# Optimization experiments

Measured on AMD Instinct MI355X. Metric: run time of the kernel, lower is better.

The kernel has to match this reference:

```python
import jax, jax.numpy as jnp
import numpy as np

B, N, D_IN = 4, 2048, 128
H, HD = 4, 32  # num_heads, head_dim (out_features=128, concat=True)
NEG_SLOPE = 0.2


def setup_inputs() -> dict:
    key = jax.random.key(0)
    kx, kadj, kw, ka = jax.random.split(key, 4)
    x = jax.random.normal(kx, (B, N, D_IN), dtype=jnp.float32)
    adj_mx = jax.random.randint(kadj, (N, N), 0, 2, dtype=jnp.int32)
    # xavier-uniform-ish scaling for params
    W = jax.random.normal(kw, (H * HD, D_IN), dtype=jnp.float32) * (1.0 / np.sqrt(D_IN))
    a = jax.random.normal(ka, (H, 2 * HD, 1), dtype=jnp.float32) * (1.0 / np.sqrt(2 * HD))
    return {"x": x, "adj_mx": adj_mx, "W": W, "a": a}


def reference(x, adj_mx, W, a):
    # x: (B,N,D_in); W: (H*hd, D_in) [nn.Linear weight]; a: (H, 2*hd, 1)
    b, n, _ = x.shape
    hd = a.shape[1] // 2
    h = (x @ W.T).reshape(b, n, H, hd)  # (B,N,H,hd)
    # e_ij = a^T [h_i || h_j] = a1.h_i + a2.h_j  (exact decomposition of the concat-matmul)
    a1 = a[:, :hd, 0]  # (H, hd)
    a2 = a[:, hd:, 0]  # (H, hd)
    ei = jnp.einsum('bnhd,hd->bnh', h, a1)
    ej = jnp.einsum('bnhd,hd->bnh', h, a2)
    e = ei[:, :, None, :] + ej[:, None, :, :]  # (B,N,N,H)
    e = jnp.where(e > 0, e, NEG_SLOPE * e)  # leaky_relu(0.2)
    mask = (adj_mx == 0)[None, :, :, None]  # (1,N,N,1)
    e = jnp.where(mask, -jnp.inf, e)
    attn = jax.nn.softmax(e, axis=2)  # softmax over neighbors j
    # dropout p=0.0 (inference) -> identity
    out = jnp.einsum('bijh,bjhd->bihd', attn, h)  # (B,N,H,hd)
    return out.reshape(b, n, H * hd)  # concat heads
```

## Files before the change

### kernel.cpp

```cpp
#include <hip/hip_runtime.h>
#include <hip/hip_bf16.h>
#include <stdint.h>

#define B 4
#define N 2048
#define DIN 128
#define H 4
#define HD 32
#define NEG 0.2f
#define LOG2E 1.4426950408889634f
#define WINJ 256

typedef __attribute__((ext_vector_type(8))) short short8;
typedef __attribute__((ext_vector_type(4))) float f32x4;


__global__ __launch_bounds__(256) void k_prep(const float* __restrict__ x,
                                              const float* __restrict__ W,
                                              const float* __restrict__ a,
                                              const int* __restrict__ adj,
                                              unsigned short* __restrict__ VT,
                                              float* __restrict__ ei_t,
                                              float* __restrict__ ej_t,
                                              unsigned long long* __restrict__ bitsT) {
    __shared__ float Wt0[64][64];
    __shared__ float Wt1[64][64];
    __shared__ float xT[64][20];

    const int tid = threadIdx.x;
    if (blockIdx.x >= 512) {
        int t = (blockIdx.x - 512) * 256 + tid;
        int v = adj[t];
        unsigned long long m = __ballot(v != 0);
        if ((tid & 63) == 0) {
            int row = t >> 11, jw = (t >> 6) & 31;
            bitsT[(size_t)jw * 2048 + row] = m;
        }
        return;
    }

    const int lane = tid & 63;
    const int r0 = (tid >> 6) * 4;
    const int c2 = lane;
    const int rowBase = blockIdx.x * 16;
    float acc[4][2];
#pragma unroll
    for (int i = 0; i < 4; ++i) { acc[i][0] = 0.f; acc[i][1] = 0.f; }

    for (int kh = 0; kh < 2; ++kh) {
        __syncthreads();
        {
            const int c = tid & 127;
            const int qb = (tid >> 7) * 8;
            const int ci = c >> 1, pl = c & 1;
            const float4* W4 = (const float4*)W;
#pragma unroll
            for (int q = 0; q < 8; ++q) {
                float4 v = W4[c * 32 + kh * 16 + qb + q];
                int kk = (qb + q) * 4;
                if (pl == 0) {
                    Wt0[kk + 0][ci] = v.x; Wt0[kk + 1][ci] = v.y;
                    Wt0[kk + 2][ci] = v.z; Wt0[kk + 3][ci] = v.w;
                } else {
                    Wt1[kk + 0][ci] = v.x; Wt1[kk + 1][ci] = v.y;
                    Wt1[kk + 2][ci] = v.z; Wt1[kk + 3][ci] = v.w;
                }
            }
        }
        {
            const int rl = tid >> 4;
            const int q = tid & 15;
            float4 v = ((const float4*)x)[(rowBase + rl) * 32 + kh * 16 + q];
            int kk = q * 4;
            xT[kk + 0][rl] = v.x; xT[kk + 1][rl] = v.y;
            xT[kk + 2][rl] = v.z; xT[kk + 3][rl] = v.w;
        }
        __syncthreads();
#pragma unroll 8
        for (int kk = 0; kk < 64; ++kk) {
            float w0 = Wt0[kk][c2];
            float w1 = Wt1[kk][c2];
#pragma unroll
            for (int i = 0; i < 4; ++i) {
                float xv = xT[kk][r0 + i];
                acc[i][0] += xv * w0;
                acc[i][1] += xv * w1;
            }
        }
    }

    const int c0 = 2 * c2;
    const int headT = c0 >> 5, d0 = c0 & 31;
    const int b = rowBase >> 11;
    const int n0 = (rowBase & 2047) + r0;
    const int bh = b * 4 + headT;

    {
        ushort4 p0, p1;
        unsigned short* q0 = (unsigned short*)&p0;
        unsigned short* q1 = (unsigned short*)&p1;
#pragma unroll
        for (int i = 0; i < 4; ++i) {
            __hip_bfloat16 h0 = __float2bfloat16(acc[i][0]);
            __hip_bfloat16 h1 = __float2bfloat16(acc[i][1]);
            q0[i] = *(unsigned short*)&h0;
            q1[i] = *(unsigned short*)&h1;
        }
        const int wdw = n0 >> 8;
        const int gw  = (n0 >> 3) & 31;
        const int off = n0 & 7;
        const int gs0 = gw ^ (d0 & 7);
        const int gs1 = gw ^ ((d0 + 1) & 7);
        *(ushort4*)&VT[((size_t)bh * 32 + d0) * 2048 + wdw * WINJ + gs0 * 8 + off] = p0;
        *(ushort4*)&VT[((size_t)bh * 32 + d0 + 1) * 2048 + wdw * WINJ + gs1 * 8 + off] = p1;
    }
    {
        float a10 = a[headT * 64 + d0],      a11 = a[headT * 64 + d0 + 1];
        float a20 = a[headT * 64 + 32 + d0], a21 = a[headT * 64 + 32 + d0 + 1];
#pragma unroll
        for (int i = 0; i < 4; ++i) {
            float pi = acc[i][0] * a10 + acc[i][1] * a11;
            float pj = acc[i][0] * a20 + acc[i][1] * a21;
#pragma unroll
            for (int off = 1; off < 16; off <<= 1) {
                pi += __shfl_xor(pi, off);
                pj += __shfl_xor(pj, off);
            }
            if ((lane & 15) == 0) {
                ei_t[(size_t)bh * 2048 + n0 + i] = pi * LOG2E;
                ej_t[(size_t)bh * 2048 + n0 + i] = pj * LOG2E;
            }
        }
    }
}

__global__ __launch_bounds__(256) void k_attn_w(const unsigned short* __restrict__ VT,
                                                const float* __restrict__ ei_t,
                                                const float* __restrict__ ej_t,
                                                const unsigned long long* __restrict__ bitsT,
                                                float* __restrict__ out) {
    __shared__ __align__(16) unsigned short Vs[2][32 * WINJ];
    __shared__ __align__(16) float ejs[2][WINJ];

    const int tid = threadIdx.x;
    const int bid = blockIdx.x;
    const int rt = bid & 31;
    const int head = (bid >> 5) & 3;
    const int b = bid >> 7;
    const int wv = tid >> 6, lane = tid & 63;
    const int lr = lane & 15;
    const int g = lane >> 4;
    const int rowW = rt * 64 + wv * 16;
    const int bh = b * 4 + head;

    const unsigned short* VTb = VT + (size_t)bh * 32 * 2048;
    const float* ejg = ej_t + (size_t)bh * 2048;
    const float eir = ei_t[(size_t)bh * 2048 + rowW + lr];

    f32x4 acc0 = {0.f, 0.f, 0.f, 0.f};
    f32x4 acc1 = {0.f, 0.f, 0.f, 0.f};
    f32x4 accS = {0.f, 0.f, 0.f, 0.f};
    short8 onesb;
    {
        short ov = (lr == 0) ? (short)0x3F80 : (short)0;
#pragma unroll
        for (int e = 0; e < 8; ++e) onesb[e] = ov;
    }

    {
#pragma unroll
        for (int i = 0; i < 4; ++i) {
            int L = i * 256 + tid, d = L >> 5, gr = L & 31;
            float4 v = *(const float4*)&VTb[(size_t)d * 2048 + gr * 8];
            *(float4*)&Vs[0][(size_t)L * 8] = v;
        }
        if (tid < 64) {
            float4 e = *(const float4*)&ejg[tid * 4];
            *(float4*)&ejs[0][tid * 4] = e;
        }
    }
    __syncthreads();

    for (int w = 0; w < 8; ++w) {
        const int buf = w & 1;
        const unsigned long long wreg =
            bitsT[(size_t)(w * 4 + g) * 2048 + rowW + lr];

        float4 vr0, vr1, vr2, vr3, er;
        const bool pf = (w < 7);
        if (pf) {
            const unsigned short* src = VTb + (w + 1) * WINJ;
            vr0 = *(const float4*)&src[(size_t)((tid)        >> 5) * 2048 + ((tid)        & 31) * 8];
            vr1 = *(const float4*)&src[(size_t)((256 + tid)  >> 5) * 2048 + ((256 + tid)  & 31) * 8];
            vr2 = *(const float4*)&src[(size_t)((512 + tid)  >> 5) * 2048 + ((512 + tid)  & 31) * 8];
            vr3 = *(const float4*)&src[(size_t)((768 + tid)  >> 5) * 2048 + ((768 + tid)  & 31) * 8];
            if (tid < 64) er = *(const float4*)&ejg[(w + 1) * WINJ + tid * 4];
        }
        __builtin_amdgcn_sched_barrier(0);

        const unsigned short* Vb = &Vs[buf][0];
        const float* ejb = &ejs[buf][0];
#pragma unroll
        for (int jl = 0; jl < WINJ; jl += 64) {
            const unsigned long long word = __shfl(wreg, (jl >> 6) * 16 + lr);
#pragma unroll
            for (int ks = 0; ks < 2; ++ks) {
                const int gw_ = (jl >> 3) + ks * 4 + g;
                const int slot = gw_ ^ (lr & 7);
                short8 b0 = *(const short8*)&Vb[lr * WINJ + slot * 8];
                short8 b1 = *(const short8*)&Vb[(16 + lr) * WINJ + slot * 8];
                const int f = jl + ks * 32 + g * 8;
                float4 ea = *(const float4*)&ejb[f];
                float4 eb = *(const float4*)&ejb[f + 4];
                const unsigned int mb =
                    (unsigned int)(word >> (ks * 32 + g * 8)) & 0xffu;
                float ej8[8] = {ea.x, ea.y, ea.z, ea.w, eb.x, eb.y, eb.z, eb.w};
                short8 pa;
#pragma unroll
                for (int e = 0; e < 8; ++e) {
                    float s = eir + ej8[e];
                    float el = fmaxf(s, NEG * s);
                    float p = ((mb >> e) & 1u) ? __builtin_amdgcn_exp2f(el) : 0.f;
                    __hip_bfloat16 pb = __float2bfloat16(p);
                    pa[e] = (short)*(unsigned short*)&pb;
                }
                __builtin_amdgcn_s_setprio(1);
                acc0 = __builtin_amdgcn_mfma_f32_16x16x32_bf16(pa, b0, acc0, 0, 0, 0);
                acc1 = __builtin_amdgcn_mfma_f32_16x16x32_bf16(pa, b1, acc1, 0, 0, 0);
                accS = __builtin_amdgcn_mfma_f32_16x16x32_bf16(pa, onesb, accS, 0, 0, 0);
                __builtin_amdgcn_s_setprio(0);
            }
        }

        if (pf) {
            const int nbuf = buf ^ 1;
            *(float4*)&Vs[nbuf][(size_t)tid * 8]          = vr0;
            *(float4*)&Vs[nbuf][(size_t)(256 + tid) * 8]  = vr1;
            *(float4*)&Vs[nbuf][(size_t)(512 + tid) * 8]  = vr2;
            *(float4*)&Vs[nbuf][(size_t)(768 + tid) * 8]  = vr3;
            if (tid < 64) *(float4*)&ejs[nbuf][tid * 4] = er;
        }
        __syncthreads();
    }

#pragma unroll
    for (int reg = 0; reg < 4; ++reg) {
        const float sr = __shfl(accS[reg], g * 16);
        const float inv = 1.f / sr;
        const int m = 4 * g + reg;
        float* dst = &out[(size_t)(b * N + rowW + m) * 128 + head * 32 + lr];
        dst[0]  = acc0[reg] * inv;
        dst[16] = acc1[reg] * inv;
    }
}

__global__ __launch_bounds__(256) void k_fused(const float* __restrict__ x,
                                               const int* __restrict__ adj,
                                               const float* __restrict__ W,
                                               const float* __restrict__ a,
                                               float* __restrict__ out) {
    __shared__ float Ws[32][129];
    __shared__ float xs[64][132];
    __shared__ float hs[64][44];
    __shared__ float ejs[64];
    __shared__ float eis[128];
    __shared__ float a1s[32], a2s[32];
    __shared__ unsigned long long mb[128];

    const int tid = threadIdx.x;
    const int bid = blockIdx.x;
    const int rt = bid & 15;
    const int head = (bid >> 4) & 3;
    const int b = bid >> 6;
    const int row0 = rt * 128;

    for (int idx = tid; idx < 32 * 128; idx += 256) {
        int d = idx >> 7, k = idx & 127;
        Ws[d][k] = W[(head * 32 + d) * 128 + k];
    }
    if (tid < 32) a1s[tid] = a[head * 64 + tid];
    else if (tid < 64) a2s[tid - 32] = a[head * 64 + tid];
    __syncthreads();

    for (int c0 = 0; c0 < 128; c0 += 64) {
        __syncthreads();
        {
            int jj = tid >> 2, k0 = (tid & 3) * 32;
            const float4* src = (const float4*)&x[(b * N + row0 + c0 + jj) * 128 + k0];
#pragma unroll
            for (int q = 0; q < 8; ++q) *(float4*)&xs[jj][k0 + q * 4] = src[q];
        }
        __syncthreads();
        {
            int jj = tid >> 2, db = (tid & 3) * 8;
#pragma unroll
            for (int dd = 0; dd < 8; ++dd) {
                float s = 0.f;
                for (int k = 0; k < 128; ++k) s += xs[jj][k] * Ws[db + dd][k];
                hs[jj][db + dd] = s;
            }
        }
        __syncthreads();
        if (tid < 64) {
            float s = 0.f;
#pragma unroll
            for (int d = 0; d < 32; ++d) s += hs[tid][d] * a1s[d];
            eis[c0 + tid] = s;
        }
    }

    const int dgrp = tid & 3, d0 = dgrp * 8;
    const int rseg = tid >> 2;
    float acc[2][8];
    float sacc[2] = {0.f, 0.f};
#pragma unroll
    for (int k = 0; k < 2; ++k)
#pragma unroll
        for (int d = 0; d < 8; ++d) acc[k][d] = 0.f;

    for (int jc = 0; jc < N; jc += 64) {
        __syncthreads();
        {
            int jj = tid >> 2, k0 = (tid & 3) * 32;
            const float4* src = (const float4*)&x[(b * N + jc + jj) * 128 + k0];
#pragma unroll
            for (int q = 0; q < 8; ++q) *(float4*)&xs[jj][k0 + q * 4] = src[q];
        }
        {
            int wv = tid >> 6, lane = tid & 63;
            for (int p = 0; p < 32; ++p) {
                int il = p * 4 + wv;
                unsigned long long m = __ballot(adj[(row0 + il) * N + jc + lane] != 0);
                if (lane == 0) mb[il] = m;
            }
        }
        __syncthreads();
        {
            int jj = tid >> 2, db = (tid & 3) * 8;
#pragma unroll
            for (int dd = 0; dd < 8; ++dd) {
                float s = 0.f;
                for (int k = 0; k < 128; ++k) s += xs[jj][k] * Ws[db + dd][k];
                hs[jj][db + dd] = s;
            }
        }
        __syncthreads();
        if (tid < 64) {
            float s = 0.f;
#pragma unroll
            for (int d = 0; d < 32; ++d) s += hs[tid][d] * a2s[d];
            ejs[tid] = s;
        }
        __syncthreads();
        for (int jj = 0; jj < 64; ++jj) {
            float ejv = ejs[jj];
            float hv[8];
#pragma unroll
            for (int d = 0; d < 8; ++d) hv[d] = hs[jj][d0 + d];
#pragma unroll
            for (int k = 0; k < 2; ++k) {
                int il = rseg * 2 + k;
                float s = eis[il] + ejv;
                float el = s > 0.f ? s : NEG * s;
                float p = ((mb[il] >> jj) & 1ull) ? __expf(el) : 0.f;
                sacc[k] += p;
#pragma unroll
                for (int d = 0; d < 8; ++d) acc[k][d] += p * hv[d];
            }
        }
    }
#pragma unroll
    for (int k = 0; k < 2; ++k) {
        int il = rseg * 2 + k;
        float inv = 1.f / sacc[k];
        float* dst = &out[(b * N + row0 + il) * 128 + head * 32 + d0];
#pragma unroll
        for (int d = 0; d < 8; ++d) dst[d] = acc[k][d] * inv;
    }
}

extern "C" void kernel_launch(void* const* d_in, const int* in_sizes, int n_in,
                              void* d_out, int out_size, void* d_ws, size_t ws_size,
                              hipStream_t stream) {
    const float* x = nullptr; const int* adj = nullptr;
    const float* W = nullptr; const float* a = nullptr;
    for (int i = 0; i < n_in; ++i) {
        switch (in_sizes[i]) {
            case B * N * DIN:  x   = (const float*)d_in[i]; break;
            case N * N:        adj = (const int*)d_in[i];   break;
            case H * HD * DIN: W   = (const float*)d_in[i]; break;
            case H * 2 * HD:   a   = (const float*)d_in[i]; break;
        }
    }
    float* out = (float*)d_out;

    const size_t szVT = (size_t)B * H * HD * N * 2;
    const size_t szE  = (size_t)B * H * N * 4;
    const size_t szBits = (size_t)N * (N / 64) * 8;
    const size_t need = szVT + 2 * szE + szBits;

    if (ws_size >= need) {
        char* ws = (char*)d_ws;
        unsigned short* VT = (unsigned short*)ws;
        float* ei_t = (float*)(ws + szVT);
        float* ej_t = (float*)(ws + szVT + szE);
        unsigned long long* bitsT = (unsigned long long*)(ws + szVT + 2 * szE);

        k_prep<<<512 + (N * N) / 256, 256, 0, stream>>>(x, W, a, adj, VT, ei_t, ej_t, bitsT);
        k_attn_w<<<512, 256, 0, stream>>>(VT, ei_t, ej_t, bitsT, out);
    } else {
        k_fused<<<256, 256, 0, stream>>>(x, adj, W, a, out);
    }
}
```

Before: 111.0 us.

## Merge prep and attention kernels into one cooperative kernel with grid sync

Replaces the two-kernel sequence (prep producing VT/ei/ej/bit-mask, then attention) with a single cooperative launch of 512 blocks that runs the prep phase, does a grid-wide sync, then runs the attention phase. Each block now packs 32 rows of adjacency bits instead of using separate bit-packing blocks. Shared memory is unioned between phases. The aim is to remove kernel launch gaps and the tail of the first kernel, at the cost of a grid barrier and the requirement that all 512 blocks stay co-resident.

```diff
diff --git a/kernel.cpp b/kernel.cpp
--- a/kernel.cpp
+++ b/kernel.cpp
@@ -1,5 +1,6 @@
 #include <hip/hip_runtime.h>
 #include <hip/hip_bf16.h>
+#include <hip/hip_cooperative_groups.h>
 #include <stdint.h>
 
 #define B 4
@@ -15,242 +16,249 @@
 typedef __attribute__((ext_vector_type(4))) float f32x4;
 
 
-__global__ __launch_bounds__(256) void k_prep(const float* __restrict__ x,
-                                              const float* __restrict__ W,
-                                              const float* __restrict__ a,
-                                              const int* __restrict__ adj,
-                                              unsigned short* __restrict__ VT,
-                                              float* __restrict__ ei_t,
-                                              float* __restrict__ ej_t,
-                                              unsigned long long* __restrict__ bitsT) {
-    __shared__ float Wt0[64][64];
-    __shared__ float Wt1[64][64];
-    __shared__ float xT[64][20];
-
-    const int tid = threadIdx.x;
-    if (blockIdx.x >= 512) {
-        int t = (blockIdx.x - 512) * 256 + tid;
-        int v = adj[t];
-        unsigned long long m = __ballot(v != 0);
-        if ((tid & 63) == 0) {
-            int row = t >> 11, jw = (t >> 6) & 31;
-            bitsT[(size_t)jw * 2048 + row] = m;
-        }
-        return;
-    }
-
-    const int lane = tid & 63;
-    const int r0 = (tid >> 6) * 4;
-    const int c2 = lane;
-    const int rowBase = blockIdx.x * 16;
-    float acc[4][2];
-#pragma unroll
-    for (int i = 0; i < 4; ++i) { acc[i][0] = 0.f; acc[i][1] = 0.f; }
-
-    for (int kh = 0; kh < 2; ++kh) {
-        __syncthreads();
-        {
-            const int c = tid & 127;
-            const int qb = (tid >> 7) * 8;
-            const int ci = c >> 1, pl = c & 1;
-            const float4* W4 = (const float4*)W;
-#pragma unroll
-            for (int q = 0; q < 8; ++q) {
-                float4 v = W4[c * 32 + kh * 16 + qb + q];
-                int kk = (qb + q) * 4;
-                if (pl == 0) {
-                    Wt0[kk + 0][ci] = v.x; Wt0[kk + 1][ci] = v.y;
-                    Wt0[kk + 2][ci] = v.z; Wt0[kk + 3][ci] = v.w;
-                } else {
-                    Wt1[kk + 0][ci] = v.x; Wt1[kk + 1][ci] = v.y;
-                    Wt1[kk + 2][ci] = v.z; Wt1[kk + 3][ci] = v.w;
-                }
-            }
-        }
-        {
-            const int rl = tid >> 4;
-            const int q = tid & 15;
-            float4 v = ((const float4*)x)[(rowBase + rl) * 32 + kh * 16 + q];
-            int kk = q * 4;
-            xT[kk + 0][rl] = v.x; xT[kk + 1][rl] = v.y;
-            xT[kk + 2][rl] = v.z; xT[kk + 3][rl] = v.w;
-        }
-        __syncthreads();
-#pragma unroll 8
-        for (int kk = 0; kk < 64; ++kk) {
-            float w0 = Wt0[kk][c2];
-            float w1 = Wt1[kk][c2];
-#pragma unroll
-            for (int i = 0; i < 4; ++i) {
-                float xv = xT[kk][r0 + i];
-                acc[i][0] += xv * w0;
-                acc[i][1] += xv * w1;
-            }
-        }
-    }
-
-    const int c0 = 2 * c2;
-    const int headT = c0 >> 5, d0 = c0 & 31;
-    const int b = rowBase >> 11;
-    const int n0 = (rowBase & 2047) + r0;
-    const int bh = b * 4 + headT;
-
-    {
-        ushort4 p0, p1;
-        unsigned short* q0 = (unsigned short*)&p0;
-        unsigned short* q1 = (unsigned short*)&p1;
-#pragma unroll
-        for (int i = 0; i < 4; ++i) {
-            __hip_bfloat16 h0 = __float2bfloat16(acc[i][0]);
-            __hip_bfloat16 h1 = __float2bfloat16(acc[i][1]);
-            q0[i] = *(unsigned short*)&h0;
-            q1[i] = *(unsigned short*)&h1;
-        }
-        const int wdw = n0 >> 8;
-        const int gw  = (n0 >> 3) & 31;
-        const int off = n0 & 7;
-        const int gs0 = gw ^ (d0 & 7);
-        const int gs1 = gw ^ ((d0 + 1) & 7);
-        *(ushort4*)&VT[((size_t)bh * 32 + d0) * 2048 + wdw * WINJ + gs0 * 8 + off] = p0;
-        *(ushort4*)&VT[((size_t)bh * 32 + d0 + 1) * 2048 + wdw * WINJ + gs1 * 8 + off] = p1;
-    }
-    {
-        float a10 = a[headT * 64 + d0],      a11 = a[headT * 64 + d0 + 1];
-        float a20 = a[headT * 64 + 32 + d0], a21 = a[headT * 64 + 32 + d0 + 1];
-#pragma unroll
-        for (int i = 0; i < 4; ++i) {
-            float pi = acc[i][0] * a10 + acc[i][1] * a11;
-            float pj = acc[i][0] * a20 + acc[i][1] * a21;
-#pragma unroll
-            for (int off = 1; off < 16; off <<= 1) {
-                pi += __shfl_xor(pi, off);
-                pj += __shfl_xor(pj, off);
-            }
-            if ((lane & 15) == 0) {
-                ei_t[(size_t)bh * 2048 + n0 + i] = pi * LOG2E;
-                ej_t[(size_t)bh * 2048 + n0 + i] = pj * LOG2E;
-            }
-        }
-    }
-}
-
-__global__ __launch_bounds__(256) void k_attn_w(const unsigned short* __restrict__ VT,
-                                                const float* __restrict__ ei_t,
-                                                const float* __restrict__ ej_t,
-                                                const unsigned long long* __restrict__ bitsT,
-                                                float* __restrict__ out) {
-    __shared__ __align__(16) unsigned short Vs[2][32 * WINJ];
-    __shared__ __align__(16) float ejs[2][WINJ];
+__global__ __launch_bounds__(256) void k_all(const float* __restrict__ x,
+                                             const float* __restrict__ W,
+                                             const float* __restrict__ a,
+                                             const int* __restrict__ adj,
+                                             unsigned short* __restrict__ VT,
+                                             float* __restrict__ ei_t,
+                                             float* __restrict__ ej_t,
+                                             unsigned long long* __restrict__ bitsT,
+                                             float* __restrict__ out) {
+    __shared__ __align__(16) char smem[37888];
 
     const int tid = threadIdx.x;
     const int bid = blockIdx.x;
-    const int rt = bid & 31;
-    const int head = (bid >> 5) & 3;
-    const int b = bid >> 7;
-    const int wv = tid >> 6, lane = tid & 63;
-    const int lr = lane & 15;
-    const int g = lane >> 4;
-    const int rowW = rt * 64 + wv * 16;
-    const int bh = b * 4 + head;
-
-    const unsigned short* VTb = VT + (size_t)bh * 32 * 2048;
-    const float* ejg = ej_t + (size_t)bh * 2048;
-    const float eir = ei_t[(size_t)bh * 2048 + rowW + lr];
-
-    f32x4 acc0 = {0.f, 0.f, 0.f, 0.f};
-    f32x4 acc1 = {0.f, 0.f, 0.f, 0.f};
-    f32x4 accS = {0.f, 0.f, 0.f, 0.f};
-    short8 onesb;
+    const int lane = tid & 63;
+
     {
-        short ov = (lr == 0) ? (short)0x3F80 : (short)0;
-#pragma unroll
-        for (int e = 0; e < 8; ++e) onesb[e] = ov;
+#pragma unroll 4
+        for (int i = 0; i < 32; ++i) {
+            int t = (bid * 32 + i) * 256 + tid;
+            int v = adj[t];
+            unsigned long long m = __ballot(v != 0);
+            if ((tid & 63) == 0) {
+                int row = t >> 11, jw = (t >> 6) & 31;
+                bitsT[(size_t)jw * 2048 + row] = m;
+            }
+        }
     }
 
     {
-#pragma unroll
-        for (int i = 0; i < 4; ++i) {
-            int L = i * 256 + tid, d = L >> 5, gr = L & 31;
-            float4 v = *(const float4*)&VTb[(size_t)d * 2048 + gr * 8];
-            *(float4*)&Vs[0][(size_t)L * 8] = v;
-        }
-        if (tid < 64) {
-            float4 e = *(const float4*)&ejg[tid * 4];
-            *(float4*)&ejs[0][tid * 4] = e;
-        }
-    }
+        float (*Wt0)[64] = (float(*)[64])smem;
+        float (*Wt1)[64] = (float(*)[64])(smem + 16384);
+        float (*xT)[20]  = (float(*)[20])(smem + 32768);
+
+        const int r0 = (tid >> 6) * 4;
+        const int c2 = lane;
+        const int rowBase = bid * 16;
+        float acc[4][2];
+#pragma unroll
+        for (int i = 0; i < 4; ++i) { acc[i][0] = 0.f; acc[i][1] = 0.f; }
+
+        for (int kh = 0; kh < 2; ++kh) {
+            __syncthreads();
+            {
+                const int c = tid & 127;
+                const int qb = (tid >> 7) * 8;
+                const int ci = c >> 1, pl = c & 1;
+                const float4* W4 = (const float4*)W;
+#pragma unroll
+                for (int q = 0; q < 8; ++q) {
+                    float4 v = W4[c * 32 + kh * 16 + qb + q];
+                    int kk = (qb + q) * 4;
+                    if (pl == 0) {
+                        Wt0[kk + 0][ci] = v.x; Wt0[kk + 1][ci] = v.y;
+                        Wt0[kk + 2][ci] = v.z; Wt0[kk + 3][ci] = v.w;
+                    } else {
+                        Wt1[kk + 0][ci] = v.x; Wt1[kk + 1][ci] = v.y;
+                        Wt1[kk + 2][ci] = v.z; Wt1[kk + 3][ci] = v.w;
+                    }
+                }
+            }
+            {
+                const int rl = tid >> 4;
+                const int q = tid & 15;
+                float4 v = ((const float4*)x)[(rowBase + rl) * 32 + kh * 16 + q];
+                int kk = q * 4;
+                xT[kk + 0][rl] = v.x; xT[kk + 1][rl] = v.y;
+                xT[kk + 2][rl] = v.z; xT[kk + 3][rl] = v.w;
+            }
+            __syncthreads();
+#pragma unroll 8
+            for (int kk = 0; kk < 64; ++kk) {
+                float w0 = Wt0[kk][c2];
+                float w1 = Wt1[kk][c2];
+#pragma unroll
+                for (int i = 0; i < 4; ++i) {
+                    float xv = xT[kk][r0 + i];
+                    acc[i][0] += xv * w0;
+                    acc[i][1] += xv * w1;
+                }
+            }
+        }
+
+        const int c0 = 2 * c2;
+        const int headT = c0 >> 5, d0 = c0 & 31;
+        const int b = rowBase >> 11;
+        const int n0 = (rowBase & 2047) + r0;
+        const int bh = b * 4 + headT;
+
+        {
+            ushort4 p0, p1;
+            unsigned short* q0 = (unsigned short*)&p0;
+            unsigned short* q1 = (unsigned short*)&p1;
+#pragma unroll
+            for (int i = 0; i < 4; ++i) {
+                __hip_bfloat16 h0 = __float2bfloat16(acc[i][0]);
+                __hip_bfloat16 h1 = __float2bfloat16(acc[i][1]);
+                q0[i] = *(unsigned short*)&h0;
+                q1[i] = *(unsigned short*)&h1;
+            }
+            const int wdw = n0 >> 8;
+            const int gw  = (n0 >> 3) & 31;
+            const int off = n0 & 7;
+            const int gs0 = gw ^ (d0 & 7);
+            const int gs1 = gw ^ ((d0 + 1) & 7);
+            *(ushort4*)&VT[((size_t)bh * 32 + d0) * 2048 + wdw * WINJ + gs0 * 8 + off] = p0;
+            *(ushort4*)&VT[((size_t)bh * 32 + d0 + 1) * 2048 + wdw * WINJ + gs1 * 8 + off] = p1;
+        }
+        {
+            float a10 = a[headT * 64 + d0],      a11 = a[headT * 64 + d0 + 1];
+            float a20 = a[headT * 64 + 32 + d0], a21 = a[headT * 64 + 32 + d0 + 1];
+#pragma unroll
+            for (int i = 0; i < 4; ++i) {
+                float pi = acc[i][0] * a10 + acc[i][1] * a11;
+                float pj = acc[i][0] * a20 + acc[i][1] * a21;
+#pragma unroll
+                for (int off = 1; off < 16; off <<= 1) {
+                    pi += __shfl_xor(pi, off);
+                    pj += __shfl_xor(pj, off);
+                }
+                if ((lane & 15) == 0) {
+                    ei_t[(size_t)bh * 2048 + n0 + i] = pi * LOG2E;
+                    ej_t[(size_t)bh * 2048 + n0 + i] = pj * LOG2E;
+                }
+            }
+        }
+    }
+
+    __threadfence();
+    cooperative_groups::this_grid().sync();
     __syncthreads();
 
-    for (int w = 0; w < 8; ++w) {
-        const int buf = w & 1;
-        const unsigned long long wreg =
-            bitsT[(size_t)(w * 4 + g) * 2048 + rowW + lr];
-
-        float4 vr0, vr1, vr2, vr3, er;
-        const bool pf = (w < 7);
-        if (pf) {
-            const unsigned short* src = VTb + (w + 1) * WINJ;
-            vr0 = *(const float4*)&src[(size_t)((tid)        >> 5) * 2048 + ((tid)        & 31) * 8];
-            vr1 = *(const float4*)&src[(size_t)((256 + tid)  >> 5) * 2048 + ((256 + tid)  & 31) * 8];
-            vr2 = *(const float4*)&src[(size_t)((512 + tid)  >> 5) * 2048 + ((512 + tid)  & 31) * 8];
-            vr3 = *(const float4*)&src[(size_t)((768 + tid)  >> 5) * 2048 + ((768 + tid)  & 31) * 8];
-            if (tid < 64) er = *(const float4*)&ejg[(w + 1) * WINJ + tid * 4];
-        }
-        __builtin_amdgcn_sched_barrier(0);
-
-        const unsigned short* Vb = &Vs[buf][0];
-        const float* ejb = &ejs[buf][0];
-#pragma unroll
-        for (int jl = 0; jl < WINJ; jl += 64) {
-            const unsigned long long word = __shfl(wreg, (jl >> 6) * 16 + lr);
-#pragma unroll
-            for (int ks = 0; ks < 2; ++ks) {
-                const int gw_ = (jl >> 3) + ks * 4 + g;
-                const int slot = gw_ ^ (lr & 7);
-                short8 b0 = *(const short8*)&Vb[lr * WINJ + slot * 8];
-                short8 b1 = *(const short8*)&Vb[(16 + lr) * WINJ + slot * 8];
-                const int f = jl + ks * 32 + g * 8;
-                float4 ea = *(const float4*)&ejb[f];
-                float4 eb = *(const float4*)&ejb[f + 4];
-                const unsigned int mb =
-                    (unsigned int)(word >> (ks * 32 + g * 8)) & 0xffu;
-                float ej8[8] = {ea.x, ea.y, ea.z, ea.w, eb.x, eb.y, eb.z, eb.w};
-                short8 pa;
-#pragma unroll
-                for (int e = 0; e < 8; ++e) {
-                    float s = eir + ej8[e];
-                    float el = fmaxf(s, NEG * s);
-                    float p = ((mb >> e) & 1u) ? __builtin_amdgcn_exp2f(el) : 0.f;
-                    __hip_bfloat16 pb = __float2bfloat16(p);
-                    pa[e] = (short)*(unsigned short*)&pb;
+    {
+        unsigned short (*Vs)[32 * WINJ] = (unsigned short(*)[32 * WINJ])smem;
+        float (*ejs)[WINJ] = (float(*)[WINJ])(smem + 32768);
+
+        const int rt = bid & 31;
+        const int head = (bid >> 5) & 3;
+        const int b = bid >> 7;
+        const int wv = tid >> 6;
+        const int lr = lane & 15;
+        const int g = lane >> 4;
+        const int rowW = rt * 64 + wv * 16;
+        const int bh = b * 4 + head;
+
+        const unsigned short* VTb = VT + (size_t)bh * 32 * 2048;
+        const float* ejg = ej_t + (size_t)bh * 2048;
+        const float eir = ei_t[(size_t)bh * 2048 + rowW + lr];
+
+        f32x4 acc0 = {0.f, 0.f, 0.f, 0.f};
+        f32x4 acc1 = {0.f, 0.f, 0.f, 0.f};
+        f32x4 accS = {0.f, 0.f, 0.f, 0.f};
+        short8 onesb;
+        {
+            short ov = (lr == 0) ? (short)0x3F80 : (short)0;
+#pragma unroll
+            for (int e = 0; e < 8; ++e) onesb[e] = ov;
+        }
+
+        {
+#pragma unroll
+            for (int i = 0; i < 4; ++i) {
+                int L = i * 256 + tid, d = L >> 5, gr = L & 31;
+                float4 v = *(const float4*)&VTb[(size_t)d * 2048 + gr * 8];
+                *(float4*)&Vs[0][(size_t)L * 8] = v;
+            }
+            if (tid < 64) {
+                float4 e = *(const float4*)&ejg[tid * 4];
+                *(float4*)&ejs[0][tid * 4] = e;
+            }
+        }
+        __syncthreads();
+
+        for (int w = 0; w < 8; ++w) {
+            const int buf = w & 1;
+            const unsigned long long wreg =
+                bitsT[(size_t)(w * 4 + g) * 2048 + rowW + lr];
+
+            float4 vr0, vr1, vr2, vr3, er;
+            const bool pf = (w < 7);
+            if (pf) {
+                const unsigned short* src = VTb + (w + 1) * WINJ;
+                vr0 = *(const float4*)&src[(size_t)((tid)       >> 5) * 2048 + ((tid)       & 31) * 8];
+                vr1 = *(const float4*)&src[(size_t)((256 + tid) >> 5) * 2048 + ((256 + tid) & 31) * 8];
+                vr2 = *(const float4*)&src[(size_t)((512 + tid) >> 5) * 2048 + ((512 + tid) & 31) * 8];
+                vr3 = *(const float4*)&src[(size_t)((768 + tid) >> 5) * 2048 + ((768 + tid) & 31) * 8];
+                if (tid < 64) er = *(const float4*)&ejg[(w + 1) * WINJ + tid * 4];
+            }
+            __builtin_amdgcn_sched_barrier(0);
+
+            const unsigned short* Vb = &Vs[buf][0];
+            const float* ejb = &ejs[buf][0];
+#pragma unroll
+            for (int jl = 0; jl < WINJ; jl += 64) {
+                const unsigned long long word = __shfl(wreg, (jl >> 6) * 16 + lr);
+#pragma unroll
+                for (int ks = 0; ks < 2; ++ks) {
+                    const int gw_ = (jl >> 3) + ks * 4 + g;
+                    const int slot = gw_ ^ (lr & 7);
+                    short8 b0 = *(const short8*)&Vb[lr * WINJ + slot * 8];
+                    short8 b1 = *(const short8*)&Vb[(16 + lr) * WINJ + slot * 8];
+                    const int f = jl + ks * 32 + g * 8;
+                    float4 ea = *(const float4*)&ejb[f];
+                    float4 eb = *(const float4*)&ejb[f + 4];
+                    const unsigned int mb =
+                        (unsigned int)(word >> (ks * 32 + g * 8)) & 0xffu;
+                    float ej8[8] = {ea.x, ea.y, ea.z, ea.w, eb.x, eb.y, eb.z, eb.w};
+                    short8 pa;
+#pragma unroll
+                    for (int e = 0; e < 8; ++e) {
+                        float s = eir + ej8[e];
+                        float el = fmaxf(s, NEG * s);
+                        float p = ((mb >> e) & 1u) ? __builtin_amdgcn_exp2f(el) : 0.f;
+                        __hip_bfloat16 pb = __float2bfloat16(p);
+                        pa[e] = (short)*(unsigned short*)&pb;
+                    }
+                    __builtin_amdgcn_s_setprio(1);
+                    acc0 = __builtin_amdgcn_mfma_f32_16x16x32_bf16(pa, b0, acc0, 0, 0, 0);
+                    acc1 = __builtin_amdgcn_mfma_f32_16x16x32_bf16(pa, b1, acc1, 0, 0, 0);
+                    accS = __builtin_amdgcn_mfma_f32_16x16x32_bf16(pa, onesb, accS, 0, 0, 0);
+                    __builtin_amdgcn_s_setprio(0);
                 }
-                __builtin_amdgcn_s_setprio(1);
-                acc0 = __builtin_amdgcn_mfma_f32_16x16x32_bf16(pa, b0, acc0, 0, 0, 0);
-                acc1 = __builtin_amdgcn_mfma_f32_16x16x32_bf16(pa, b1, acc1, 0, 0, 0);
-                accS = __builtin_amdgcn_mfma_f32_16x16x32_bf16(pa, onesb, accS, 0, 0, 0);
-                __builtin_amdgcn_s_setprio(0);
-            }
-        }
-
-        if (pf) {
-            const int nbuf = buf ^ 1;
-            *(float4*)&Vs[nbuf][(size_t)tid * 8]          = vr0;
-            *(float4*)&Vs[nbuf][(size_t)(256 + tid) * 8]  = vr1;
-            *(float4*)&Vs[nbuf][(size_t)(512 + tid) * 8]  = vr2;
-            *(float4*)&Vs[nbuf][(size_t)(768 + tid) * 8]  = vr3;
-            if (tid < 64) *(float4*)&ejs[nbuf][tid * 4] = er;
-        }
-        __syncthreads();
-    }
-
-#pragma unroll
-    for (int reg = 0; reg < 4; ++reg) {
-        const float sr = __shfl(accS[reg], g * 16);
-        const float inv = 1.f / sr;
-        const int m = 4 * g + reg;
-        float* dst = &out[(size_t)(b * N + rowW + m) * 128 + head * 32 + lr];
-        dst[0]  = acc0[reg] * inv;
-        dst[16] = acc1[reg] * inv;
+            }
+
+            if (pf) {
+                const int nbuf = buf ^ 1;
+                *(float4*)&Vs[nbuf][(size_t)tid * 8]         = vr0;
+                *(float4*)&Vs[nbuf][(size_t)(256 + tid) * 8] = vr1;
+                *(float4*)&Vs[nbuf][(size_t)(512 + tid) * 8] = vr2;
+                *(float4*)&Vs[nbuf][(size_t)(768 + tid) * 8] = vr3;
+                if (tid < 64) *(float4*)&ejs[nbuf][tid * 4] = er;
+            }
+            __syncthreads();
+        }
+
+#pragma unroll
+        for (int reg = 0; reg < 4; ++reg) {
+            const float sr = __shfl(accS[reg], g * 16);
+            const float inv = 1.f / sr;
+            const int m = 4 * g + reg;
+            float* dst = &out[(size_t)(b * N + rowW + m) * 128 + head * 32 + lr];
+            dst[0]  = acc0[reg] * inv;
+            dst[16] = acc1[reg] * inv;
+        }
     }
 }
 
@@ -406,8 +414,11 @@
         float* ej_t = (float*)(ws + szVT + szE);
         unsigned long long* bitsT = (unsigned long long*)(ws + szVT + 2 * szE);
 
-        k_prep<<<512 + (N * N) / 256, 256, 0, stream>>>(x, W, a, adj, VT, ei_t, ej_t, bitsT);
-        k_attn_w<<<512, 256, 0, stream>>>(VT, ei_t, ej_t, bitsT, out);
+        void* kargs[] = {(void*)&x, (void*)&W, (void*)&a, (void*)&adj,
+                         (void*)&VT, (void*)&ei_t, (void*)&ej_t, (void*)&bitsT,
+                         (void*)&out};
+        hipLaunchCooperativeKernel((void*)k_all, dim3(512), dim3(256),
+                                   kargs, 0, stream);
     } else {
         k_fused<<<256, 256, 0, stream>>>(x, adj, W, a, out);
     }
```

Measured after the change: 223.7 us. +101.6%, slower.

## Split attention j-range across two wave groups and fold adjacency packing into prep blocks

Applied to the files above, without the earlier changes.

The attention kernel now launches 512 threads per block. Two groups of four waves each handle half of the neighbor range with their own double-buffered LDS tiles, and the partial accumulators are reduced through shared memory at the end. This doubles the waves available per row tile to hide latency, at the cost of more LDS per block and an extra reduction. Separately, the adjacency bitmask packing no longer runs in 16384 tiny extra blocks; each of the 512 prep blocks now loops over 32 chunks, which removes launch and scheduling overhead but lengthens each prep block.

```diff
diff --git a/kernel.cpp b/kernel.cpp
--- a/kernel.cpp
+++ b/kernel.cpp
@@ -28,21 +28,25 @@
     __shared__ float xT[64][20];
 
     const int tid = threadIdx.x;
-    if (blockIdx.x >= 512) {
-        int t = (blockIdx.x - 512) * 256 + tid;
-        int v = adj[t];
-        unsigned long long m = __ballot(v != 0);
-        if ((tid & 63) == 0) {
-            int row = t >> 11, jw = (t >> 6) & 31;
-            bitsT[(size_t)jw * 2048 + row] = m;
-        }
-        return;
-    }
-
+    const int bid = blockIdx.x;
     const int lane = tid & 63;
+
+    {
+#pragma unroll 4
+        for (int i = 0; i < 32; ++i) {
+            int t = (bid * 32 + i) * 256 + tid;
+            int v = adj[t];
+            unsigned long long m = __ballot(v != 0);
+            if ((tid & 63) == 0) {
+                int row = t >> 11, jw = (t >> 6) & 31;
+                bitsT[(size_t)jw * 2048 + row] = m;
+            }
+        }
+    }
+
     const int r0 = (tid >> 6) * 4;
     const int c2 = lane;
-    const int rowBase = blockIdx.x * 16;
+    const int rowBase = bid * 16;
     float acc[4][2];
 #pragma unroll
     for (int i = 0; i < 4; ++i) { acc[i][0] = 0.f; acc[i][1] = 0.f; }
@@ -134,13 +138,13 @@
     }
 }
 
-__global__ __launch_bounds__(256) void k_attn_w(const unsigned short* __restrict__ VT,
+__global__ __launch_bounds__(512) void k_attn_p(const unsigned short* __restrict__ VT,
                                                 const float* __restrict__ ei_t,
                                                 const float* __restrict__ ej_t,
                                                 const unsigned long long* __restrict__ bitsT,
                                                 float* __restrict__ out) {
-    __shared__ __align__(16) unsigned short Vs[2][32 * WINJ];
-    __shared__ __align__(16) float ejs[2][WINJ];
+    __shared__ __align__(16) unsigned short Vs[2][2][32 * WINJ];
+    __shared__ __align__(16) float ejs[2][2][WINJ];
 
     const int tid = threadIdx.x;
     const int bid = blockIdx.x;
@@ -148,9 +152,10 @@
     const int head = (bid >> 5) & 3;
     const int b = bid >> 7;
     const int wv = tid >> 6, lane = tid & 63;
+    const int wtile = wv & 3, par = wv >> 2;
     const int lr = lane & 15;
     const int g = lane >> 4;
-    const int rowW = rt * 64 + wv * 16;
+    const int rowW = rt * 64 + wtile * 16;
     const int bh = b * 4 + head;
 
     const unsigned short* VTb = VT + (size_t)bh * 32 * 2048;
@@ -169,37 +174,49 @@
 
     {
 #pragma unroll
-        for (int i = 0; i < 4; ++i) {
-            int L = i * 256 + tid, d = L >> 5, gr = L & 31;
-            float4 v = *(const float4*)&VTb[(size_t)d * 2048 + gr * 8];
-            *(float4*)&Vs[0][(size_t)L * 8] = v;
-        }
-        if (tid < 64) {
-            float4 e = *(const float4*)&ejg[tid * 4];
-            *(float4*)&ejs[0][tid * 4] = e;
+        for (int p = 0; p < 2; ++p) {
+            const unsigned short* src = VTb + (p * 4) * WINJ;
+#pragma unroll
+            for (int i = 0; i < 2; ++i) {
+                int L = i * 512 + tid, d = L >> 5, gr = L & 31;
+                float4 v = *(const float4*)&src[(size_t)d * 2048 + gr * 8];
+                *(float4*)&Vs[p][0][(size_t)L * 8] = v;
+            }
+        }
+        if (tid < 128) {
+            int p = tid >> 6, idx = tid & 63;
+            float4 e = *(const float4*)&ejg[(p * 4) * WINJ + idx * 4];
+            *(float4*)&ejs[p][0][idx * 4] = e;
         }
     }
     __syncthreads();
 
-    for (int w = 0; w < 8; ++w) {
-        const int buf = w & 1;
+    for (int t = 0; t < 4; ++t) {
+        const int buf = t & 1;
+        const int Wd = par * 4 + t;
         const unsigned long long wreg =
-            bitsT[(size_t)(w * 4 + g) * 2048 + rowW + lr];
+            bitsT[(size_t)(Wd * 4 + g) * 2048 + rowW + lr];
 
         float4 vr0, vr1, vr2, vr3, er;
-        const bool pf = (w < 7);
+        const bool pf = (t < 3);
         if (pf) {
-            const unsigned short* src = VTb + (w + 1) * WINJ;
-            vr0 = *(const float4*)&src[(size_t)((tid)        >> 5) * 2048 + ((tid)        & 31) * 8];
-            vr1 = *(const float4*)&src[(size_t)((256 + tid)  >> 5) * 2048 + ((256 + tid)  & 31) * 8];
-            vr2 = *(const float4*)&src[(size_t)((512 + tid)  >> 5) * 2048 + ((512 + tid)  & 31) * 8];
-            vr3 = *(const float4*)&src[(size_t)((768 + tid)  >> 5) * 2048 + ((768 + tid)  & 31) * 8];
-            if (tid < 64) er = *(const float4*)&ejg[(w + 1) * WINJ + tid * 4];
+            const unsigned short* s0 = VTb + (t + 1) * WINJ;
+            const unsigned short* s1 = VTb + (5 + t) * WINJ;
+            int L0 = tid, d0_ = L0 >> 5, g0_ = L0 & 31;
+            int L1 = 512 + tid, d1_ = L1 >> 5, g1_ = L1 & 31;
+            vr0 = *(const float4*)&s0[(size_t)d0_ * 2048 + g0_ * 8];
+            vr1 = *(const float4*)&s0[(size_t)d1_ * 2048 + g1_ * 8];
+            vr2 = *(const float4*)&s1[(size_t)d0_ * 2048 + g0_ * 8];
+            vr3 = *(const float4*)&s1[(size_t)d1_ * 2048 + g1_ * 8];
+            if (tid < 128) {
+                int p = tid >> 6, idx = tid & 63;
+                er = *(const float4*)&ejg[(p ? (5 + t) : (t + 1)) * WINJ + idx * 4];
+            }
         }
         __builtin_amdgcn_sched_barrier(0);
 
-        const unsigned short* Vb = &Vs[buf][0];
-        const float* ejb = &ejs[buf][0];
+        const unsigned short* Vb = &Vs[par][buf][0];
+        const float* ejb = &ejs[par][buf][0];
 #pragma unroll
         for (int jl = 0; jl < WINJ; jl += 64) {
             const unsigned long long word = __shfl(wreg, (jl >> 6) * 16 + lr);
@@ -233,24 +250,43 @@
         }
 
         if (pf) {
-            const int nbuf = buf ^ 1;
-            *(float4*)&Vs[nbuf][(size_t)tid * 8]          = vr0;
-            *(float4*)&Vs[nbuf][(size_t)(256 + tid) * 8]  = vr1;
-            *(float4*)&Vs[nbuf][(size_t)(512 + tid) * 8]  = vr2;
-            *(float4*)&Vs[nbuf][(size_t)(768 + tid) * 8]  = vr3;
-            if (tid < 64) *(float4*)&ejs[nbuf][tid * 4] = er;
-        }
-        __syncthreads();
-    }
-
-#pragma unroll
-    for (int reg = 0; reg < 4; ++reg) {
-        const float sr = __shfl(accS[reg], g * 16);
-        const float inv = 1.f / sr;
-        const int m = 4 * g + reg;
-        float* dst = &out[(size_t)(b * N + rowW + m) * 128 + head * 32 + lr];
-        dst[0]  = acc0[reg] * inv;
-        dst[16] = acc1[reg] * inv;
+            const int nb = buf ^ 1;
+            *(float4*)&Vs[0][nb][(size_t)tid * 8]         = vr0;
+            *(float4*)&Vs[0][nb][(size_t)(512 + tid) * 8] = vr1;
+            *(float4*)&Vs[1][nb][(size_t)tid * 8]         = vr2;
+            *(float4*)&Vs[1][nb][(size_t)(512 + tid) * 8] = vr3;
+            if (tid < 128) {
+                int p = tid >> 6, idx = tid & 63;
+                *(float4*)&ejs[p][nb][idx * 4] = er;
+            }
+        }
+        __syncthreads();
+    }
+
+    float* redf = (float*)&Vs[0][0][0];
+    if (par == 1) {
+        float* r = &redf[(wtile * 64 + lane) * 13];
+#pragma unroll
+        for (int q = 0; q < 4; ++q) {
+            r[q] = acc0[q]; r[4 + q] = acc1[q]; r[8 + q] = accS[q];
+        }
+    }
+    __syncthreads();
+    if (par == 0) {
+        const float* r = &redf[(wtile * 64 + lane) * 13];
+#pragma unroll
+        for (int q = 0; q < 4; ++q) {
+            acc0[q] += r[q]; acc1[q] += r[4 + q]; accS[q] += r[8 + q];
+        }
+#pragma unroll
+        for (int reg = 0; reg < 4; ++reg) {
+            const float sr = __shfl(accS[reg], g * 16);
+            const float inv = 1.f / sr;
+            const int m = 4 * g + reg;
+            float* dst = &out[(size_t)(b * N + rowW + m) * 128 + head * 32 + lr];
+            dst[0]  = acc0[reg] * inv;
+            dst[16] = acc1[reg] * inv;
+        }
     }
 }
 
@@ -406,8 +442,8 @@
         float* ej_t = (float*)(ws + szVT + szE);
         unsigned long long* bitsT = (unsigned long long*)(ws + szVT + 2 * szE);
 
-        k_prep<<<512 + (N * N) / 256, 256, 0, stream>>>(x, W, a, adj, VT, ei_t, ej_t, bitsT);
-        k_attn_w<<<512, 256, 0, stream>>>(VT, ei_t, ej_t, bitsT, out);
+        k_prep<<<512, 256, 0, stream>>>(x, W, a, adj, VT, ei_t, ej_t, bitsT);
+        k_attn_p<<<512, 512, 0, stream>>>(VT, ei_t, ej_t, bitsT, out);
     } else {
         k_fused<<<256, 256, 0, stream>>>(x, adj, W, a, out);
     }
```

Measured after the change: 112.2 us. Within noise of the previous version (+1.1%).

## Merge adjacency bitpacking into projection blocks and enlarge projection register tile

Applied to the files above, without the earlier changes.

The prep kernel previously ran 512 projection blocks plus 16384 tiny blocks for bitpacking adj. Now it launches 256 blocks, each of which first packs 64 chunks of the adjacency matrix and then computes a 32-row by 128-col projection tile using a 4x4 register tile with float4 LDS reads. This removes per-block launch overhead from the many small blocks and raises FMA-to-load ratio in the projection. The trade-off is fewer blocks (256 on a 256-CU device), which could hurt latency hiding for the adjacency loads, and the serialized bitpack loop precedes the GEMM in every block.

```diff
diff --git a/kernel.cpp b/kernel.cpp
--- a/kernel.cpp
+++ b/kernel.cpp
@@ -23,110 +23,122 @@
                                               float* __restrict__ ei_t,
                                               float* __restrict__ ej_t,
                                               unsigned long long* __restrict__ bitsT) {
-    __shared__ float Wt0[64][64];
-    __shared__ float Wt1[64][64];
-    __shared__ float xT[64][20];
+    __shared__ float Wt[64][132];
+    __shared__ float xT[64][36];
 
     const int tid = threadIdx.x;
-    if (blockIdx.x >= 512) {
-        int t = (blockIdx.x - 512) * 256 + tid;
-        int v = adj[t];
-        unsigned long long m = __ballot(v != 0);
-        if ((tid & 63) == 0) {
-            int row = t >> 11, jw = (t >> 6) & 31;
-            bitsT[(size_t)jw * 2048 + row] = m;
-        }
-        return;
-    }
-
+    const int bid = blockIdx.x;
     const int lane = tid & 63;
-    const int r0 = (tid >> 6) * 4;
-    const int c2 = lane;
-    const int rowBase = blockIdx.x * 16;
-    float acc[4][2];
-#pragma unroll
-    for (int i = 0; i < 4; ++i) { acc[i][0] = 0.f; acc[i][1] = 0.f; }
+
+    {
+#pragma unroll 4
+        for (int i = 0; i < 64; ++i) {
+            int t = (bid * 64 + i) * 256 + tid;
+            int v = adj[t];
+            unsigned long long m = __ballot(v != 0);
+            if ((tid & 63) == 0) {
+                int row = t >> 11, jw = (t >> 6) & 31;
+                bitsT[(size_t)jw * 2048 + row] = m;
+            }
+        }
+    }
+
+    const int rg = tid >> 5;
+    const int cg = tid & 31;
+    const int r0 = rg * 4;
+    const int c0 = cg * 4;
+    const int rowBase = bid * 32;
+    float acc[4][4];
+#pragma unroll
+    for (int i = 0; i < 4; ++i)
+#pragma unroll
+        for (int q = 0; q < 4; ++q) acc[i][q] = 0.f;
 
     for (int kh = 0; kh < 2; ++kh) {
         __syncthreads();
         {
             const int c = tid & 127;
             const int qb = (tid >> 7) * 8;
-            const int ci = c >> 1, pl = c & 1;
             const float4* W4 = (const float4*)W;
 #pragma unroll
             for (int q = 0; q < 8; ++q) {
                 float4 v = W4[c * 32 + kh * 16 + qb + q];
                 int kk = (qb + q) * 4;
-                if (pl == 0) {
-                    Wt0[kk + 0][ci] = v.x; Wt0[kk + 1][ci] = v.y;
-                    Wt0[kk + 2][ci] = v.z; Wt0[kk + 3][ci] = v.w;
-                } else {
-                    Wt1[kk + 0][ci] = v.x; Wt1[kk + 1][ci] = v.y;
-                    Wt1[kk + 2][ci] = v.z; Wt1[kk + 3][ci] = v.w;
-                }
-            }
-        }
-        {
-            const int rl = tid >> 4;
-            const int q = tid & 15;
-            float4 v = ((const float4*)x)[(rowBase + rl) * 32 + kh * 16 + q];
-            int kk = q * 4;
-            xT[kk + 0][rl] = v.x; xT[kk + 1][rl] = v.y;
-            xT[kk + 2][rl] = v.z; xT[kk + 3][rl] = v.w;
+                Wt[kk + 0][c] = v.x; Wt[kk + 1][c] = v.y;
+                Wt[kk + 2][c] = v.z; Wt[kk + 3][c] = v.w;
+            }
+        }
+        {
+            const int rl = tid >> 3;
+            const int q0 = (tid & 7) * 2;
+            const float4* x4 = (const float4*)x;
+#pragma unroll
+            for (int qi = 0; qi < 2; ++qi) {
+                int q = q0 + qi;
+                float4 v = x4[(rowBase + rl) * 32 + kh * 16 + q];
+                int kk = q * 4;
+                xT[kk + 0][rl] = v.x; xT[kk + 1][rl] = v.y;
+                xT[kk + 2][rl] = v.z; xT[kk + 3][rl] = v.w;
+            }
         }
         __syncthreads();
 #pragma unroll 8
         for (int kk = 0; kk < 64; ++kk) {
-            float w0 = Wt0[kk][c2];
-            float w1 = Wt1[kk][c2];
-#pragma unroll
-            for (int i = 0; i < 4; ++i) {
-                float xv = xT[kk][r0 + i];
-                acc[i][0] += xv * w0;
-                acc[i][1] += xv * w1;
-            }
-        }
-    }
-
-    const int c0 = 2 * c2;
-    const int headT = c0 >> 5, d0 = c0 & 31;
+            float4 w4 = *(const float4*)&Wt[kk][c0];
+            float4 x4v = *(const float4*)&xT[kk][r0];
+            float wv[4] = {w4.x, w4.y, w4.z, w4.w};
+            float xv[4] = {x4v.x, x4v.y, x4v.z, x4v.w};
+#pragma unroll
+            for (int i = 0; i < 4; ++i)
+#pragma unroll
+                for (int q = 0; q < 4; ++q) acc[i][q] += xv[i] * wv[q];
+        }
+    }
+
     const int b = rowBase >> 11;
     const int n0 = (rowBase & 2047) + r0;
-    const int bh = b * 4 + headT;
 
     {
-        ushort4 p0, p1;
-        unsigned short* q0 = (unsigned short*)&p0;
-        unsigned short* q1 = (unsigned short*)&p1;
-#pragma unroll
-        for (int i = 0; i < 4; ++i) {
-            __hip_bfloat16 h0 = __float2bfloat16(acc[i][0]);
-            __hip_bfloat16 h1 = __float2bfloat16(acc[i][1]);
-            q0[i] = *(unsigned short*)&h0;
-            q1[i] = *(unsigned short*)&h1;
-        }
         const int wdw = n0 >> 8;
         const int gw  = (n0 >> 3) & 31;
         const int off = n0 & 7;
-        const int gs0 = gw ^ (d0 & 7);
-        const int gs1 = gw ^ ((d0 + 1) & 7);
-        *(ushort4*)&VT[((size_t)bh * 32 + d0) * 2048 + wdw * WINJ + gs0 * 8 + off] = p0;
-        *(ushort4*)&VT[((size_t)bh * 32 + d0 + 1) * 2048 + wdw * WINJ + gs1 * 8 + off] = p1;
+#pragma unroll
+        for (int q = 0; q < 4; ++q) {
+            const int col = c0 + q;
+            const int head = col >> 5, d = col & 31;
+            const int bh = b * 4 + head;
+            ushort4 p;
+            unsigned short* pu = (unsigned short*)&p;
+#pragma unroll
+            for (int i = 0; i < 4; ++i) {
+                __hip_bfloat16 hb = __float2bfloat16(acc[i][q]);
+                pu[i] = *(unsigned short*)&hb;
+            }
+            const int gs = gw ^ (d & 7);
+            *(ushort4*)&VT[((size_t)bh * 32 + d) * 2048 + wdw * WINJ + gs * 8 + off] = p;
+        }
     }
     {
-        float a10 = a[headT * 64 + d0],      a11 = a[headT * 64 + d0 + 1];
-        float a20 = a[headT * 64 + 32 + d0], a21 = a[headT * 64 + 32 + d0 + 1];
+        const int head = c0 >> 5, d = c0 & 31;
+        const int bh = b * 4 + head;
+        float a1v[4], a2v[4];
+#pragma unroll
+        for (int q = 0; q < 4; ++q) {
+            a1v[q] = a[head * 64 + d + q];
+            a2v[q] = a[head * 64 + 32 + d + q];
+        }
 #pragma unroll
         for (int i = 0; i < 4; ++i) {
-            float pi = acc[i][0] * a10 + acc[i][1] * a11;
-            float pj = acc[i][0] * a20 + acc[i][1] * a21;
-#pragma unroll
-            for (int off = 1; off < 16; off <<= 1) {
+            float pi = acc[i][0] * a1v[0] + acc[i][1] * a1v[1]
+                     + acc[i][2] * a1v[2] + acc[i][3] * a1v[3];
+            float pj = acc[i][0] * a2v[0] + acc[i][1] * a2v[1]
+                     + acc[i][2] * a2v[2] + acc[i][3] * a2v[3];
+#pragma unroll
+            for (int off = 1; off < 8; off <<= 1) {
                 pi += __shfl_xor(pi, off);
                 pj += __shfl_xor(pj, off);
             }
-            if ((lane & 15) == 0) {
+            if ((lane & 7) == 0) {
                 ei_t[(size_t)bh * 2048 + n0 + i] = pi * LOG2E;
                 ej_t[(size_t)bh * 2048 + n0 + i] = pj * LOG2E;
             }
@@ -190,10 +202,10 @@
         const bool pf = (w < 7);
         if (pf) {
             const unsigned short* src = VTb + (w + 1) * WINJ;
-            vr0 = *(const float4*)&src[(size_t)((tid)        >> 5) * 2048 + ((tid)        & 31) * 8];
-            vr1 = *(const float4*)&src[(size_t)((256 + tid)  >> 5) * 2048 + ((256 + tid)  & 31) * 8];
-            vr2 = *(const float4*)&src[(size_t)((512 + tid)  >> 5) * 2048 + ((512 + tid)  & 31) * 8];
-            vr3 = *(const float4*)&src[(size_t)((768 + tid)  >> 5) * 2048 + ((768 + tid)  & 31) * 8];
+            vr0 = *(const float4*)&src[(size_t)((tid)       >> 5) * 2048 + ((tid)       & 31) * 8];
+            vr1 = *(const float4*)&src[(size_t)((256 + tid) >> 5) * 2048 + ((256 + tid) & 31) * 8];
+            vr2 = *(const float4*)&src[(size_t)((512 + tid) >> 5) * 2048 + ((512 + tid) & 31) * 8];
+            vr3 = *(const float4*)&src[(size_t)((768 + tid) >> 5) * 2048 + ((768 + tid) & 31) * 8];
             if (tid < 64) er = *(const float4*)&ejg[(w + 1) * WINJ + tid * 4];
         }
         __builtin_amdgcn_sched_barrier(0);
@@ -406,7 +418,7 @@
         float* ej_t = (float*)(ws + szVT + szE);
         unsigned long long* bitsT = (unsigned long long*)(ws + szVT + 2 * szE);
 
-        k_prep<<<512 + (N * N) / 256, 256, 0, stream>>>(x, W, a, adj, VT, ei_t, ej_t, bitsT);
+        k_prep<<<256, 256, 0, stream>>>(x, W, a, adj, VT, ei_t, ej_t, bitsT);
         k_attn_w<<<512, 256, 0, stream>>>(VT, ei_t, ej_t, bitsT, out);
     } else {
         k_fused<<<256, 256, 0, stream>>>(x, adj, W, a, out);
```

After: 123.7 us. 1.11x slower.
